# Optimization experiments

Measured on AMD Instinct MI355X. Metric: run time of the kernel, lower is better.

Reference implementation:

```python
import jax, jax.numpy as jnp
import numpy as np

B, S, HID = 1, 2048, 4096
H, HKV = 32, 8
D = HID // H          # 128
G = H // HKV          # 4 query heads per kv head (GQA)


def setup_inputs() -> dict:
    key = jax.random.key(0)
    ks = jax.random.split(key, 5)
    hidden_states = jax.random.normal(ks[0], (B, S, HID), dtype=jnp.float32)
    # additive causal mask: 0 on/below diagonal, large negative above
    causal = jnp.tril(jnp.ones((S, S), dtype=bool))
    attention_mask = jnp.where(causal, 0.0, -1e9).astype(jnp.float32)[None, None]
    sc = 0.02
    wq = jax.random.normal(ks[1], (HID, H * D), dtype=jnp.float32) * sc
    wk = jax.random.normal(ks[2], (HID, HKV * D), dtype=jnp.float32) * sc
    wv = jax.random.normal(ks[3], (HID, HKV * D), dtype=jnp.float32) * sc
    wo = jax.random.normal(ks[4], (H * D, HID), dtype=jnp.float32) * sc
    return {"hidden_states": hidden_states, "attention_mask": attention_mask,
            "wq": wq, "wk": wk, "wv": wv, "wo": wo}


def reference(hidden_states, attention_mask, wq, wk, wv, wo):
    # projections (lora_rank=0 path: plain dense, no bias)
    q = hidden_states @ wq                      # [B,S,H*D]
    k = hidden_states @ wk                      # [B,S,HKV*D]
    v = hidden_states @ wv                      # [B,S,HKV*D]
    # split heads; group query heads by their kv head: head h -> (h//G, h%G)
    q = q.reshape(B, S, HKV, G, D).transpose(0, 2, 3, 1, 4)   # [B,HKV,G,S,D]
    k = k.reshape(B, S, HKV, D).transpose(0, 2, 1, 3)          # [B,HKV,S,D]
    v = v.reshape(B, S, HKV, D).transpose(0, 2, 1, 3)          # [B,HKV,S,D]
    scale = 1.0 / jnp.sqrt(jnp.float32(D))
    # explicit S x S scores (as in source), with GQA kv broadcast over G
    scores = jnp.einsum('bkgsd,bktd->bkgst', q, k) * scale     # [B,HKV,G,S,S]
    scores = scores + attention_mask[:, :, None]               # broadcast over G
    probs = jax.nn.softmax(scores, axis=-1)
    attn = jnp.einsum('bkgst,bktd->bkgsd', probs, v)           # [B,HKV,G,S,D]
    attn = attn.transpose(0, 3, 1, 2, 4).reshape(B, S, H * D)  # [B,S,H*D]
    return attn @ wo                                           # [B,S,HID]
```

## Files before the change

kernel.cpp:

```cpp
#include <hip/hip_runtime.h>
#include <hip/hip_bf16.h>

#define S_LEN 2048
#define HID 4096
#define NH 32
#define NKV 8
#define HD 128
#define LDQKV 6144

typedef __bf16 bf16x8 __attribute__((ext_vector_type(8)));
typedef __bf16 bf16x4 __attribute__((ext_vector_type(4)));
typedef float f32x4 __attribute__((ext_vector_type(4)));

#define GLD16(gp, lp)                                                                   \
    __builtin_amdgcn_global_load_lds((const __attribute__((address_space(1))) void*)(gp), \
                                     (__attribute__((address_space(3))) void*)(lp), 16, 0, 0)

#define MFMA_BF16(a, b, c) __builtin_amdgcn_mfma_f32_16x16x32_bf16((a), (b), (c), 0, 0, 0)

__global__ void cast_bf16_kernel(const float* __restrict__ x, __bf16* __restrict__ y, int n) {
    int i = (blockIdx.x * blockDim.x + threadIdx.x) * 4;
    if (i < n) {
        float4 v = *reinterpret_cast<const float4*>(x + i);
        bf16x4 o;
        o.x = (__bf16)v.x; o.y = (__bf16)v.y; o.z = (__bf16)v.z; o.w = (__bf16)v.w;
        *reinterpret_cast<bf16x4*>(y + i) = o;
    }
}

__global__ void transpose_cast_kernel(const float* __restrict__ W, __bf16* __restrict__ WT,
                                      int K, int N, float scale) {
    __shared__ float tile[32][33];
    int bx = blockIdx.x;
    int by = blockIdx.y;
    int tx = threadIdx.x;
    int ty = threadIdx.y;
    int n = bx * 32 + tx;
#pragma unroll
    for (int i = 0; i < 4; i++) {
        int k = by * 32 + ty + i * 8;
        tile[ty + i * 8][tx] = W[(size_t)k * N + n];
    }
    __syncthreads();
    int k2 = by * 32 + tx;
#pragma unroll
    for (int i = 0; i < 4; i++) {
        int n2 = bx * 32 + ty + i * 8;
        WT[(size_t)n2 * K + k2] = (__bf16)(tile[tx][ty + i * 8] * scale);
    }
}

__global__ void transpose_bf16_kernel(const __bf16* __restrict__ V, int ldin,
                                      __bf16* __restrict__ VT, int ldout) {
    __shared__ __bf16 tile[32][33];
    int bx = blockIdx.x;
    int by = blockIdx.y;
    int tx = threadIdx.x;
    int ty = threadIdx.y;
#pragma unroll
    for (int i = 0; i < 4; i++)
        tile[ty + i * 8][tx] = V[(size_t)(by * 32 + ty + i * 8) * ldin + bx * 32 + tx];
    __syncthreads();
#pragma unroll
    for (int i = 0; i < 4; i++)
        VT[(size_t)(bx * 32 + ty + i * 8) * ldout + by * 32 + tx] = tile[tx][ty + i * 8];
}

template <int BM, int BN, typename OUT_T>
__global__ __launch_bounds__(256, 2) void gemm_pipe2_kernel(const __bf16* __restrict__ A, int lda,
                                                            const __bf16* __restrict__ BT, int ldb,
                                                            OUT_T* __restrict__ C, int ldc, int K) {
    constexpr int NFA = BM / 32;
    constexpr int NFB = BN / 32;
    constexpr int AR = BM / 32;
    constexpr int BR = BN / 32;
    __shared__ __bf16 As[2][BM * 64];
    __shared__ __bf16 Bs[2][BN * 64];
    const int n0 = blockIdx.x * BN;
    const int m0 = blockIdx.y * BM;
    const int tid = threadIdx.x;
    const int lane = tid & 63, quad = lane >> 4, l16 = lane & 15;
    const int wave = tid >> 6;
    const int wm = (wave >> 1) * (BM / 2);
    const int wn = (wave & 1) * (BN / 2);

    f32x4 acc[NFA][NFB] = {};

    auto STAGE = [&](int b, int kb) {
#pragma unroll
        for (int r = 0; r < AR; r++) {
            int c = r * 256 + tid;
            int row = c >> 3;
            int col8 = (c & 7) ^ (row & 7);
            GLD16(&A[(size_t)(m0 + row) * lda + kb + col8 * 8], &As[b][c * 8]);
        }
#pragma unroll
        for (int r = 0; r < BR; r++) {
            int c = r * 256 + tid;
            int row = c >> 3;
            int col8 = (c & 7) ^ (row & 7);
            GLD16(&BT[(size_t)(n0 + row) * ldb + kb + col8 * 8], &Bs[b][c * 8]);
        }
    };

    auto READ_SET = [&](const __bf16* Asb, const __bf16* Bsb, int kk,
                        bf16x8 (&fa)[NFA], bf16x8 (&fb)[NFB]) {
        int slot = ((kk * 4 + quad) ^ (l16 & 7)) * 8;
#pragma unroll
        for (int i = 0; i < NFA; i++)
            fa[i] = *reinterpret_cast<const bf16x8*>(&Asb[(wm + i * 16 + l16) * 64 + slot]);
#pragma unroll
        for (int j = 0; j < NFB; j++)
            fb[j] = *reinterpret_cast<const bf16x8*>(&Bsb[(wn + j * 16 + l16) * 64 + slot]);
    };

    auto MF = [&](bf16x8 (&fa)[NFA], bf16x8 (&fb)[NFB]) {
        __builtin_amdgcn_s_setprio(1);
#pragma unroll
        for (int i = 0; i < NFA; i++)
#pragma unroll
            for (int j = 0; j < NFB; j++)
                acc[i][j] = MFMA_BF16(fa[i], fb[j], acc[i][j]);
        __builtin_amdgcn_s_setprio(0);
    };

    auto WAIT_SET = [&]() {
        if constexpr (NFA + NFB == 8) {
            asm volatile("s_waitcnt lgkmcnt(8)" ::: "memory");
        } else if constexpr (NFA + NFB == 10) {
            asm volatile("s_waitcnt lgkmcnt(10)" ::: "memory");
        } else {
            asm volatile("s_waitcnt lgkmcnt(12)" ::: "memory");
        }
        __builtin_amdgcn_sched_barrier(0);
    };

    const int nk = K >> 6;
    bf16x8 fa0[NFA], fb0[NFB], fa1[NFA], fb1[NFB];

    STAGE(0, 0);
    STAGE(1, 64);
    if constexpr (AR + BR == 8) {
        asm volatile("s_waitcnt vmcnt(8)" ::: "memory");
    } else {
        asm volatile("s_waitcnt vmcnt(10)" ::: "memory");
    }
    __builtin_amdgcn_sched_barrier(0);
    __builtin_amdgcn_s_barrier();
    READ_SET(As[0], Bs[0], 0, fa0, fb0);

    for (int kt = 0; kt < nk; ++kt) {
        const int cur = kt & 1;
        READ_SET(As[cur], Bs[cur], 1, fa1, fb1);
        WAIT_SET();
        MF(fa0, fb0);
        if (kt + 1 < nk) {
            asm volatile("s_waitcnt vmcnt(0)" ::: "memory");
            __builtin_amdgcn_sched_barrier(0);
            __builtin_amdgcn_s_barrier();
            READ_SET(As[cur ^ 1], Bs[cur ^ 1], 0, fa0, fb0);
            WAIT_SET();
        } else {
            asm volatile("s_waitcnt lgkmcnt(0)" ::: "memory");
            __builtin_amdgcn_sched_barrier(0);
        }
        if (kt + 2 < nk) {
            __builtin_amdgcn_s_barrier();
            STAGE(cur, (kt + 2) << 6);
        }
        MF(fa1, fb1);
    }

#pragma unroll
    for (int i = 0; i < NFA; i++)
#pragma unroll
        for (int j = 0; j < NFB; j++)
#pragma unroll
            for (int r = 0; r < 4; r++) {
                int row = m0 + wm + i * 16 + quad * 4 + r;
                int col = n0 + wn + j * 16 + l16;
                C[(size_t)row * ldc + col] = (OUT_T)acc[i][j][r];
            }
}

__global__ __launch_bounds__(256) void attn_kernel(const __bf16* __restrict__ QKV,
                                                   const __bf16* __restrict__ VT,
                                                   __bf16* __restrict__ Ao,
                                                   __bf16* __restrict__ Opart,
                                                   float* __restrict__ Lp) {
    __shared__ __bf16 Ks[64 * 128];
    __shared__ __bf16 Vs[128 * 64];
    __shared__ __bf16 Pl[4][2][16 * 72];
    int x = blockIdx.x;
    int qt, c;
    if (x < 32) { qt = 31 - (x >> 1); c = x & 1; }
    else        { qt = 47 - x;        c = 0;     }
    int hp = blockIdx.y;
    int kvh = hp >> 1;
    int h0 = kvh * 4 + (hp & 1) * 2;
    int t0 = c ? 16 : 0;
    int t1 = c ? qt : min(qt, 15);
    int tid = threadIdx.x;
    int wave = tid >> 6, lane = tid & 63, quad = lane >> 4, l16 = lane & 15;
    int wq = qt * 64 + wave * 16;
    const __bf16* Kb = QKV + HID + (size_t)kvh * HD;
    const __bf16* Vt = VT + (size_t)kvh * HD * S_LEN;

    bf16x8 qf[2][4];
#pragma unroll
    for (int h = 0; h < 2; h++)
#pragma unroll
        for (int ks = 0; ks < 4; ks++)
            qf[h][ks] = *reinterpret_cast<const bf16x8*>(
                &QKV[(size_t)(wq + l16) * LDQKV + (h0 + h) * HD + ks * 32 + quad * 8]);

    bf16x8 ones;
#pragma unroll
    for (int j = 0; j < 8; j++) ones[j] = (__bf16)1.0f;

    f32x4 acc_o[2][8] = {};
    f32x4 lacc[2] = {};

    for (int t = t0; t <= t1; t++) {
        int kv0 = t << 6;
        bool diag = (t == qt);
        __syncthreads();
#pragma unroll
        for (int i = 0; i < 4; i++) {
            int cc = i * 256 + tid;
            int row = cc >> 4, sub = cc & 15;
            int col8 = sub ^ (row & 15);
            GLD16(&Kb[(size_t)(kv0 + row) * LDQKV + col8 * 8], &Ks[cc * 8]);
        }
#pragma unroll
        for (int i = 0; i < 4; i++) {
            int cc = i * 256 + tid;
            int row = cc >> 3, sub = cc & 7;
            int col8 = sub ^ (row & 7);
            GLD16(&Vt[(size_t)row * S_LEN + kv0 + col8 * 8], &Vs[cc * 8]);
        }
        __syncthreads();

        f32x4 sacc[2][4] = {};
#pragma unroll
        for (int ks = 0; ks < 4; ks++) {
            bf16x8 kf[4];
#pragma unroll
            for (int n = 0; n < 4; n++) {
                int row = n * 16 + l16;
                int sub = (ks * 4 + quad) ^ l16;
                kf[n] = *reinterpret_cast<const bf16x8*>(&Ks[row * 128 + sub * 8]);
            }
#pragma unroll
            for (int n = 0; n < 4; n++) {
                sacc[0][n] = MFMA_BF16(qf[0][ks], kf[n], sacc[0][n]);
                sacc[1][n] = MFMA_BF16(qf[1][ks], kf[n], sacc[1][n]);
            }
        }
#pragma unroll
        for (int h = 0; h < 2; h++) {
            __bf16* Pw = Pl[wave][h];
#pragma unroll
            for (int r = 0; r < 4; r++) {
                int row = wq + quad * 4 + r;
#pragma unroll
                for (int n = 0; n < 4; n++) {
                    float v = sacc[h][n][r];
                    if (diag) {
                        int col = kv0 + n * 16 + l16;
                        if (col > row) v = -1e30f;
                    }
                    Pw[(quad * 4 + r) * 72 + n * 16 + l16] =
                        (__bf16)__builtin_amdgcn_exp2f(v);
                }
            }
        }
#pragma unroll
        for (int ks = 0; ks < 2; ks++) {
            bf16x8 pf0 = *reinterpret_cast<const bf16x8*>(
                &Pl[wave][0][l16 * 72 + ks * 32 + quad * 8]);
            bf16x8 pf1 = *reinterpret_cast<const bf16x8*>(
                &Pl[wave][1][l16 * 72 + ks * 32 + quad * 8]);
            lacc[0] = MFMA_BF16(pf0, ones, lacc[0]);
            lacc[1] = MFMA_BF16(pf1, ones, lacc[1]);
#pragma unroll
            for (int dn = 0; dn < 8; dn++) {
                int row = dn * 16 + l16;
                int sub = (ks * 4 + quad) ^ (row & 7);
                bf16x8 vf = *reinterpret_cast<const bf16x8*>(&Vs[row * 64 + sub * 8]);
                acc_o[0][dn] = MFMA_BF16(pf0, vf, acc_o[0][dn]);
                acc_o[1][dn] = MFMA_BF16(pf1, vf, acc_o[1][dn]);
            }
        }
    }

    if (qt < 16) {
#pragma unroll
        for (int h = 0; h < 2; h++) {
            float rl[4];
#pragma unroll
            for (int r = 0; r < 4; r++) rl[r] = 1.0f / lacc[h][r];
#pragma unroll
            for (int dn = 0; dn < 8; dn++)
#pragma unroll
                for (int r = 0; r < 4; r++) {
                    int row = wq + quad * 4 + r;
                    int col = (h0 + h) * HD + dn * 16 + l16;
                    Ao[(size_t)row * HID + col] = (__bf16)(acc_o[h][dn][r] * rl[r]);
                }
        }
    } else {
        int s = (qt - 16) * 2 + c;
#pragma unroll
        for (int h = 0; h < 2; h++) {
            size_t base = ((size_t)(h0 + h) * 32 + s) * 64 + wave * 16;
#pragma unroll
            for (int dn = 0; dn < 8; dn++)
#pragma unroll
                for (int r = 0; r < 4; r++)
                    Opart[(base + quad * 4 + r) * 128 + dn * 16 + l16] =
                        (__bf16)acc_o[h][dn][r];
            if (l16 == 0) {
#pragma unroll
                for (int r = 0; r < 4; r++)
                    Lp[base + quad * 4 + r] = lacc[h][r];
            }
        }
    }
}

__global__ __launch_bounds__(256) void attn_combine(const __bf16* __restrict__ Opart,
                                                    const float* __restrict__ Lp,
                                                    __bf16* __restrict__ Ao) {
    int qt = 16 + (int)blockIdx.x;
    int h = blockIdx.y;
    int tid = threadIdx.x;
    size_t b0 = ((size_t)h * 32 + (qt - 16) * 2) * 64;
    size_t b1 = b0 + 64;
#pragma unroll 4
    for (int i = 0; i < 32; i++) {
        int el = i * 256 + tid;
        int rl = el >> 7, col = el & 127;
        float l = Lp[b0 + rl] + Lp[b1 + rl];
        float O = (float)Opart[(b0 + rl) * 128 + col] + (float)Opart[(b1 + rl) * 128 + col];
        int row = qt * 64 + rl;
        Ao[(size_t)row * HID + h * HD + col] = (__bf16)(O / l);
    }
}

extern "C" void kernel_launch(void* const* d_in, const int* in_sizes, int n_in,
                              void* d_out, int out_size, void* d_ws, size_t ws_size,
                              hipStream_t stream) {
    const float* hs = (const float*)d_in[0];
    const float* wq = (const float*)d_in[2];
    const float* wk = (const float*)d_in[3];
    const float* wv = (const float*)d_in[4];
    const float* wo = (const float*)d_in[5];
    float* out = (float*)d_out;

    char* ws = (char*)d_ws;
    __bf16* WqkvT = (__bf16*)(ws + (size_t)0);
    __bf16* Opart = (__bf16*)(ws + (size_t)0);
    float*  Lp    = (float*)(ws + ((size_t)20 << 20));
    __bf16* Xb    = (__bf16*)(ws + ((size_t)48 << 20));
    __bf16* QKV   = (__bf16*)(ws + ((size_t)64 << 20));
    __bf16* VTg   = (__bf16*)(ws + ((size_t)88 << 20));
    __bf16* Ab    = Xb;

    const int nX = S_LEN * HID;
    const float SC2 = 0.12751743f;

    cast_bf16_kernel<<<nX / 4 / 256, 256, 0, stream>>>(hs, Xb, nX);
    transpose_cast_kernel<<<dim3(128, 128), dim3(32, 8), 0, stream>>>(wq, WqkvT, HID, HID, SC2);
    transpose_cast_kernel<<<dim3(32, 128), dim3(32, 8), 0, stream>>>(
        wk, WqkvT + (size_t)4096 * HID, HID, NKV * HD, 1.0f);
    transpose_cast_kernel<<<dim3(32, 128), dim3(32, 8), 0, stream>>>(
        wv, WqkvT + (size_t)5120 * HID, HID, NKV * HD, 1.0f);
    gemm_pipe2_kernel<128, 192, __bf16><<<dim3(LDQKV / 192, S_LEN / 128), 256, 0, stream>>>(
        Xb, HID, WqkvT, HID, QKV, LDQKV, HID);
    transpose_bf16_kernel<<<dim3(32, 64), dim3(32, 8), 0, stream>>>(
        QKV + 5120, LDQKV, VTg, S_LEN);
    attn_kernel<<<dim3(48, 16), 256, 0, stream>>>(QKV, VTg, Ab, Opart, Lp);
    attn_combine<<<dim3(16, 32), 256, 0, stream>>>(Opart, Lp, Ab);
    transpose_cast_kernel<<<dim3(128, 128), dim3(32, 8), 0, stream>>>(wo, WqkvT, HID, HID, 1.0f);
    gemm_pipe2_kernel<128, 128, float><<<dim3(HID / 128, S_LEN / 128), 256, 0, stream>>>(
        Ab, HID, WqkvT, HID, out, HID, HID);
}
```

Before: 481.0 us.

## Fuse prep casts into one kernel and switch GEMMs to three-stage K=32 pipeline

Merges the hidden-state cast and the three weight transpose-casts into a single launch that dispatches on block index, removing several kernel launches. Both GEMMs now use a triple-buffered shared-memory pipeline with K-tiles of 32 instead of double-buffered tiles of 64. This keeps more loads in flight with a new swizzle and waitcnt schedule. The trade-off is more barriers per unit of K and shorter MFMA bursts per barrier.

```diff
diff --git a/kernel.cpp b/kernel.cpp
--- a/kernel.cpp
+++ b/kernel.cpp
@@ -18,13 +18,52 @@
 
 #define MFMA_BF16(a, b, c) __builtin_amdgcn_mfma_f32_16x16x32_bf16((a), (b), (c), 0, 0, 0)
 
-__global__ void cast_bf16_kernel(const float* __restrict__ x, __bf16* __restrict__ y, int n) {
-    int i = (blockIdx.x * blockDim.x + threadIdx.x) * 4;
-    if (i < n) {
-        float4 v = *reinterpret_cast<const float4*>(x + i);
+#define SC2_CONST 0.12751743f
+
+__global__ __launch_bounds__(256) void prep_kernel(const float* __restrict__ hs,
+                                                   __bf16* __restrict__ Xb,
+                                                   const float* __restrict__ wq,
+                                                   const float* __restrict__ wk,
+                                                   const float* __restrict__ wv,
+                                                   __bf16* __restrict__ WqkvT) {
+    __shared__ float tile[32][33];
+    const int b = blockIdx.x;
+    const int tid = threadIdx.x;
+    if (b < 8192) {
+        int i = (b * 256 + tid) * 4;
+        float4 v = *reinterpret_cast<const float4*>(hs + i);
         bf16x4 o;
         o.x = (__bf16)v.x; o.y = (__bf16)v.y; o.z = (__bf16)v.z; o.w = (__bf16)v.w;
-        *reinterpret_cast<bf16x4*>(y + i) = o;
+        *reinterpret_cast<bf16x4*>(Xb + i) = o;
+        return;
+    }
+    const float* W;
+    __bf16* WT;
+    int N, bx, by, bb;
+    float scale;
+    if (b < 24576) {
+        bb = b - 8192;  W = wq; WT = WqkvT;                         N = HID;  scale = SC2_CONST;
+        bx = bb & 127; by = bb >> 7;
+    } else if (b < 28672) {
+        bb = b - 24576; W = wk; WT = WqkvT + (size_t)4096 * HID;    N = 1024; scale = 1.0f;
+        bx = bb & 31;  by = bb >> 5;
+    } else {
+        bb = b - 28672; W = wv; WT = WqkvT + (size_t)5120 * HID;    N = 1024; scale = 1.0f;
+        bx = bb & 31;  by = bb >> 5;
+    }
+    const int tx = tid & 31, ty = tid >> 5;
+    const int n = bx * 32 + tx;
+#pragma unroll
+    for (int i = 0; i < 4; i++) {
+        int k = by * 32 + ty + i * 8;
+        tile[ty + i * 8][tx] = W[(size_t)k * N + n];
+    }
+    __syncthreads();
+    const int k2 = by * 32 + tx;
+#pragma unroll
+    for (int i = 0; i < 4; i++) {
+        int n2 = bx * 32 + ty + i * 8;
+        WT[(size_t)n2 * HID + k2] = (__bf16)(tile[tx][ty + i * 8] * scale);
     }
 }
 
@@ -67,15 +106,16 @@
 }
 
 template <int BM, int BN, typename OUT_T>
-__global__ __launch_bounds__(256, 2) void gemm_pipe2_kernel(const __bf16* __restrict__ A, int lda,
+__global__ __launch_bounds__(256, 2) void gemm_pipe3_kernel(const __bf16* __restrict__ A, int lda,
                                                             const __bf16* __restrict__ BT, int ldb,
                                                             OUT_T* __restrict__ C, int ldc, int K) {
     constexpr int NFA = BM / 32;
     constexpr int NFB = BN / 32;
-    constexpr int AR = BM / 32;
-    constexpr int BR = BN / 32;
-    __shared__ __bf16 As[2][BM * 64];
-    __shared__ __bf16 Bs[2][BN * 64];
+    constexpr int AR = BM / 64;
+    constexpr int BR = BN / 64;
+    constexpr int INFLT = AR + BR;
+    __shared__ __bf16 As[3][BM * 32];
+    __shared__ __bf16 Bs[3][BN * 32];
     const int n0 = blockIdx.x * BN;
     const int m0 = blockIdx.y * BM;
     const int tid = threadIdx.x;
@@ -86,32 +126,32 @@
 
     f32x4 acc[NFA][NFB] = {};
 
-    auto STAGE = [&](int b, int kb) {
+    auto STAGE = [&](int b, int kt) {
+        int kb = kt << 5;
 #pragma unroll
         for (int r = 0; r < AR; r++) {
             int c = r * 256 + tid;
-            int row = c >> 3;
-            int col8 = (c & 7) ^ (row & 7);
-            GLD16(&A[(size_t)(m0 + row) * lda + kb + col8 * 8], &As[b][c * 8]);
+            int row = c >> 2;
+            int gcol = (c & 3) ^ ((row >> 1) & 3);
+            GLD16(&A[(size_t)(m0 + row) * lda + kb + gcol * 8], &As[b][c * 8]);
         }
 #pragma unroll
         for (int r = 0; r < BR; r++) {
             int c = r * 256 + tid;
-            int row = c >> 3;
-            int col8 = (c & 7) ^ (row & 7);
-            GLD16(&BT[(size_t)(n0 + row) * ldb + kb + col8 * 8], &Bs[b][c * 8]);
+            int row = c >> 2;
+            int gcol = (c & 3) ^ ((row >> 1) & 3);
+            GLD16(&BT[(size_t)(n0 + row) * ldb + kb + gcol * 8], &Bs[b][c * 8]);
         }
     };
 
-    auto READ_SET = [&](const __bf16* Asb, const __bf16* Bsb, int kk,
-                        bf16x8 (&fa)[NFA], bf16x8 (&fb)[NFB]) {
-        int slot = ((kk * 4 + quad) ^ (l16 & 7)) * 8;
+    auto READ_SET = [&](int b, bf16x8 (&fa)[NFA], bf16x8 (&fb)[NFB]) {
+        int slot = (quad ^ ((l16 >> 1) & 3)) * 8;
 #pragma unroll
         for (int i = 0; i < NFA; i++)
-            fa[i] = *reinterpret_cast<const bf16x8*>(&Asb[(wm + i * 16 + l16) * 64 + slot]);
+            fa[i] = *reinterpret_cast<const bf16x8*>(&As[b][(wm + i * 16 + l16) * 32 + slot]);
 #pragma unroll
         for (int j = 0; j < NFB; j++)
-            fb[j] = *reinterpret_cast<const bf16x8*>(&Bsb[(wn + j * 16 + l16) * 64 + slot]);
+            fb[j] = *reinterpret_cast<const bf16x8*>(&Bs[b][(wn + j * 16 + l16) * 32 + slot]);
     };
 
     auto MF = [&](bf16x8 (&fa)[NFA], bf16x8 (&fb)[NFB]) {
@@ -124,51 +164,41 @@
         __builtin_amdgcn_s_setprio(0);
     };
 
-    auto WAIT_SET = [&]() {
-        if constexpr (NFA + NFB == 8) {
-            asm volatile("s_waitcnt lgkmcnt(8)" ::: "memory");
-        } else if constexpr (NFA + NFB == 10) {
-            asm volatile("s_waitcnt lgkmcnt(10)" ::: "memory");
-        } else {
-            asm volatile("s_waitcnt lgkmcnt(12)" ::: "memory");
-        }
-        __builtin_amdgcn_sched_barrier(0);
-    };
-
-    const int nk = K >> 6;
+    const int nk = K >> 5;
     bf16x8 fa0[NFA], fb0[NFB], fa1[NFA], fb1[NFB];
 
-    STAGE(0, 0);
-    STAGE(1, 64);
-    if constexpr (AR + BR == 8) {
-        asm volatile("s_waitcnt vmcnt(8)" ::: "memory");
-    } else {
-        asm volatile("s_waitcnt vmcnt(10)" ::: "memory");
-    }
+    STAGE(0, 0); STAGE(1, 1); STAGE(2, 2);
+    if constexpr (INFLT == 5) asm volatile("s_waitcnt vmcnt(10)" ::: "memory");
+    else                      asm volatile("s_waitcnt vmcnt(8)" ::: "memory");
     __builtin_amdgcn_sched_barrier(0);
     __builtin_amdgcn_s_barrier();
-    READ_SET(As[0], Bs[0], 0, fa0, fb0);
-
-    for (int kt = 0; kt < nk; ++kt) {
-        const int cur = kt & 1;
-        READ_SET(As[cur], Bs[cur], 1, fa1, fb1);
-        WAIT_SET();
-        MF(fa0, fb0);
+    READ_SET(0, fa0, fb0);
+
+    auto ITER = [&](int kt, bf16x8 (&Ac)[NFA], bf16x8 (&Bc)[NFB],
+                    bf16x8 (&An)[NFA], bf16x8 (&Bn)[NFB]) {
         if (kt + 1 < nk) {
-            asm volatile("s_waitcnt vmcnt(0)" ::: "memory");
+            if (kt + 2 < nk) {
+                if constexpr (INFLT == 5)
+                    asm volatile("s_waitcnt lgkmcnt(0) vmcnt(5)" ::: "memory");
+                else
+                    asm volatile("s_waitcnt lgkmcnt(0) vmcnt(4)" ::: "memory");
+            } else {
+                asm volatile("s_waitcnt lgkmcnt(0) vmcnt(0)" ::: "memory");
+            }
             __builtin_amdgcn_sched_barrier(0);
             __builtin_amdgcn_s_barrier();
-            READ_SET(As[cur ^ 1], Bs[cur ^ 1], 0, fa0, fb0);
-            WAIT_SET();
+            if (kt + 3 < nk) STAGE(kt % 3, kt + 3);
+            READ_SET((kt + 1) % 3, An, Bn);
         } else {
             asm volatile("s_waitcnt lgkmcnt(0)" ::: "memory");
             __builtin_amdgcn_sched_barrier(0);
         }
-        if (kt + 2 < nk) {
-            __builtin_amdgcn_s_barrier();
-            STAGE(cur, (kt + 2) << 6);
-        }
-        MF(fa1, fb1);
+        MF(Ac, Bc);
+    };
+
+    for (int kt = 0; kt < nk; kt += 2) {
+        ITER(kt, fa0, fb0, fa1, fb1);
+        ITER(kt + 1, fa1, fb1, fa0, fb0);
     }
 
 #pragma unroll
@@ -367,22 +397,14 @@
     __bf16* VTg   = (__bf16*)(ws + ((size_t)88 << 20));
     __bf16* Ab    = Xb;
 
-    const int nX = S_LEN * HID;
-    const float SC2 = 0.12751743f;
-
-    cast_bf16_kernel<<<nX / 4 / 256, 256, 0, stream>>>(hs, Xb, nX);
-    transpose_cast_kernel<<<dim3(128, 128), dim3(32, 8), 0, stream>>>(wq, WqkvT, HID, HID, SC2);
-    transpose_cast_kernel<<<dim3(32, 128), dim3(32, 8), 0, stream>>>(
-        wk, WqkvT + (size_t)4096 * HID, HID, NKV * HD, 1.0f);
-    transpose_cast_kernel<<<dim3(32, 128), dim3(32, 8), 0, stream>>>(
-        wv, WqkvT + (size_t)5120 * HID, HID, NKV * HD, 1.0f);
-    gemm_pipe2_kernel<128, 192, __bf16><<<dim3(LDQKV / 192, S_LEN / 128), 256, 0, stream>>>(
+    prep_kernel<<<32768, 256, 0, stream>>>(hs, Xb, wq, wk, wv, WqkvT);
+    gemm_pipe3_kernel<128, 192, __bf16><<<dim3(LDQKV / 192, S_LEN / 128), 256, 0, stream>>>(
         Xb, HID, WqkvT, HID, QKV, LDQKV, HID);
     transpose_bf16_kernel<<<dim3(32, 64), dim3(32, 8), 0, stream>>>(
         QKV + 5120, LDQKV, VTg, S_LEN);
     attn_kernel<<<dim3(48, 16), 256, 0, stream>>>(QKV, VTg, Ab, Opart, Lp);
     attn_combine<<<dim3(16, 32), 256, 0, stream>>>(Opart, Lp, Ab);
     transpose_cast_kernel<<<dim3(128, 128), dim3(32, 8), 0, stream>>>(wo, WqkvT, HID, HID, 1.0f);
-    gemm_pipe2_kernel<128, 128, float><<<dim3(HID / 128, S_LEN / 128), 256, 0, stream>>>(
+    gemm_pipe3_kernel<128, 128, float><<<dim3(HID / 128, S_LEN / 128), 256, 0, stream>>>(
         Ab, HID, WqkvT, HID, out, HID, HID);
 }
```

Measured after the change: 515.9 us. 7.2% more time.

## Prefetch next KV tile into registers and merge prep kernels into one launch

Applied to the files above, without the earlier changes.

The attention loop now loads the next K/V tile into registers while MFMAs run on the current tile, then writes it to LDS between two barriers. This replaces the synchronous global_load_lds path and is meant to hide global memory latency. Separately, the bf16 cast of the activations and the three weight transpose-casts are merged into one launch to cut launch overhead. The prefetch holds more registers, which could lower occupancy, and adds an extra barrier per iteration.

```diff
diff --git a/kernel.cpp b/kernel.cpp
--- a/kernel.cpp
+++ b/kernel.cpp
@@ -18,13 +18,52 @@
 
 #define MFMA_BF16(a, b, c) __builtin_amdgcn_mfma_f32_16x16x32_bf16((a), (b), (c), 0, 0, 0)
 
-__global__ void cast_bf16_kernel(const float* __restrict__ x, __bf16* __restrict__ y, int n) {
-    int i = (blockIdx.x * blockDim.x + threadIdx.x) * 4;
-    if (i < n) {
-        float4 v = *reinterpret_cast<const float4*>(x + i);
+#define SC2_CONST 0.12751743f
+
+__global__ __launch_bounds__(256) void prep_kernel(const float* __restrict__ hs,
+                                                   __bf16* __restrict__ Xb,
+                                                   const float* __restrict__ wq,
+                                                   const float* __restrict__ wk,
+                                                   const float* __restrict__ wv,
+                                                   __bf16* __restrict__ WqkvT) {
+    __shared__ float tile[32][33];
+    const int b = blockIdx.x;
+    const int tid = threadIdx.x;
+    if (b < 8192) {
+        int i = (b * 256 + tid) * 4;
+        float4 v = *reinterpret_cast<const float4*>(hs + i);
         bf16x4 o;
         o.x = (__bf16)v.x; o.y = (__bf16)v.y; o.z = (__bf16)v.z; o.w = (__bf16)v.w;
-        *reinterpret_cast<bf16x4*>(y + i) = o;
+        *reinterpret_cast<bf16x4*>(Xb + i) = o;
+        return;
+    }
+    const float* W;
+    __bf16* WT;
+    int N, bx, by, bb;
+    float scale;
+    if (b < 24576) {
+        bb = b - 8192;  W = wq; WT = WqkvT;                         N = HID;  scale = SC2_CONST;
+        bx = bb & 127; by = bb >> 7;
+    } else if (b < 28672) {
+        bb = b - 24576; W = wk; WT = WqkvT + (size_t)4096 * HID;    N = 1024; scale = 1.0f;
+        bx = bb & 31;  by = bb >> 5;
+    } else {
+        bb = b - 28672; W = wv; WT = WqkvT + (size_t)5120 * HID;    N = 1024; scale = 1.0f;
+        bx = bb & 31;  by = bb >> 5;
+    }
+    const int tx = tid & 31, ty = tid >> 5;
+    const int n = bx * 32 + tx;
+#pragma unroll
+    for (int i = 0; i < 4; i++) {
+        int k = by * 32 + ty + i * 8;
+        tile[ty + i * 8][tx] = W[(size_t)k * N + n];
+    }
+    __syncthreads();
+    const int k2 = by * 32 + tx;
+#pragma unroll
+    for (int i = 0; i < 4; i++) {
+        int n2 = bx * 32 + ty + i * 8;
+        WT[(size_t)n2 * HID + k2] = (__bf16)(tile[tx][ty + i * 8] * scale);
     }
 }
 
@@ -221,25 +260,43 @@
     f32x4 acc_o[2][8] = {};
     f32x4 lacc[2] = {};
 
-    for (int t = t0; t <= t1; t++) {
+    bf16x8 kreg[4], vreg[4];
+    auto LOADREG = [&](int t) {
         int kv0 = t << 6;
-        bool diag = (t == qt);
-        __syncthreads();
 #pragma unroll
         for (int i = 0; i < 4; i++) {
             int cc = i * 256 + tid;
             int row = cc >> 4, sub = cc & 15;
             int col8 = sub ^ (row & 15);
-            GLD16(&Kb[(size_t)(kv0 + row) * LDQKV + col8 * 8], &Ks[cc * 8]);
+            kreg[i] = *reinterpret_cast<const bf16x8*>(
+                &Kb[(size_t)(kv0 + row) * LDQKV + col8 * 8]);
         }
 #pragma unroll
         for (int i = 0; i < 4; i++) {
             int cc = i * 256 + tid;
             int row = cc >> 3, sub = cc & 7;
             int col8 = sub ^ (row & 7);
-            GLD16(&Vt[(size_t)row * S_LEN + kv0 + col8 * 8], &Vs[cc * 8]);
-        }
-        __syncthreads();
+            vreg[i] = *reinterpret_cast<const bf16x8*>(
+                &Vt[(size_t)row * S_LEN + kv0 + col8 * 8]);
+        }
+    };
+    auto WRITELDS = [&]() {
+#pragma unroll
+        for (int i = 0; i < 4; i++)
+            *reinterpret_cast<bf16x8*>(&Ks[(i * 256 + tid) * 8]) = kreg[i];
+#pragma unroll
+        for (int i = 0; i < 4; i++)
+            *reinterpret_cast<bf16x8*>(&Vs[(i * 256 + tid) * 8]) = vreg[i];
+    };
+
+    LOADREG(t0);
+    WRITELDS();
+    __syncthreads();
+
+    for (int t = t0; t <= t1; t++) {
+        int kv0 = t << 6;
+        bool diag = (t == qt);
+        if (t < t1) LOADREG(t + 1);
 
         f32x4 sacc[2][4] = {};
 #pragma unroll
@@ -292,6 +349,10 @@
                 acc_o[1][dn] = MFMA_BF16(pf1, vf, acc_o[1][dn]);
             }
         }
+
+        __syncthreads();
+        if (t < t1) WRITELDS();
+        __syncthreads();
     }
 
     if (qt < 16) {
@@ -367,15 +428,7 @@
     __bf16* VTg   = (__bf16*)(ws + ((size_t)88 << 20));
     __bf16* Ab    = Xb;
 
-    const int nX = S_LEN * HID;
-    const float SC2 = 0.12751743f;
-
-    cast_bf16_kernel<<<nX / 4 / 256, 256, 0, stream>>>(hs, Xb, nX);
-    transpose_cast_kernel<<<dim3(128, 128), dim3(32, 8), 0, stream>>>(wq, WqkvT, HID, HID, SC2);
-    transpose_cast_kernel<<<dim3(32, 128), dim3(32, 8), 0, stream>>>(
-        wk, WqkvT + (size_t)4096 * HID, HID, NKV * HD, 1.0f);
-    transpose_cast_kernel<<<dim3(32, 128), dim3(32, 8), 0, stream>>>(
-        wv, WqkvT + (size_t)5120 * HID, HID, NKV * HD, 1.0f);
+    prep_kernel<<<32768, 256, 0, stream>>>(hs, Xb, wq, wk, wv, WqkvT);
     gemm_pipe2_kernel<128, 192, __bf16><<<dim3(LDQKV / 192, S_LEN / 128), 256, 0, stream>>>(
         Xb, HID, WqkvT, HID, QKV, LDQKV, HID);
     transpose_bf16_kernel<<<dim3(32, 64), dim3(32, 8), 0, stream>>>(
```

New measurement: 483.6 us. About the same (+0.5%).
